# Optimization experiments

Measured on AMD Instinct MI355X. Metric: run time of the kernel, lower is better.

## Reference

```python
import jax, jax.numpy as jnp
import numpy as np

B, N, G, E = 4, 8192, 512, 512
D = 3 * E  # fused channel dim = 1536
BN_EPS = 1e-5


def setup_inputs() -> dict:
    key = jax.random.key(0)
    ks = jax.random.split(key, 8)
    f32 = jnp.float32
    return {
        "xyz": jax.random.normal(ks[0], (B, N, 3), f32),
        "centers": jax.random.normal(ks[1], (B, G, 3), f32),
        "H4": jax.random.normal(ks[2], (B, G, E), f32),
        "H8": jax.random.normal(ks[3], (B, G, E), f32),
        "H12": jax.random.normal(ks[4], (B, G, E), f32),
        "w1": jax.random.normal(ks[5], (512, D), f32) * 0.02,
        "b1": jnp.zeros((512,), f32),
        "g1": jnp.ones((512,), f32),
        "be1": jnp.zeros((512,), f32),
        "m1": jnp.zeros((512,), f32),
        "v1": jnp.ones((512,), f32),
        "w2": jax.random.normal(ks[6], (512, 512), f32) * 0.02,
        "b2": jnp.zeros((512,), f32),
        "g2": jnp.ones((512,), f32),
        "be2": jnp.zeros((512,), f32),
        "m2": jnp.zeros((512,), f32),
        "v2": jnp.ones((512,), f32),
    }


def _bn(x, gamma, beta, mean, var):
    # BatchNorm1d, eval mode with running stats (per-channel, last axis)
    return (x - mean) * jax.lax.rsqrt(var + BN_EPS) * gamma + beta


def reference(xyz, centers, H4, H8, H12,
              w1, b1, g1, be1, m1, v1,
              w2, b2, g2, be2, m2, v2):
    fused = jnp.concatenate([H4, H8, H12], axis=-1)  # [B,G,D]
    # squared pairwise distances [B,N,G]
    d = (jnp.sum(xyz * xyz, axis=-1, keepdims=True)
         + jnp.sum(centers * centers, axis=-1)[:, None, :]
         - 2.0 * jnp.einsum('bnc,bgc->bng', xyz, centers))
    neg_d3, idx = jax.lax.top_k(-d, 3)  # 3 smallest distances, ascending
    d3 = -neg_d3  # [B,N,3]
    recip = 1.0 / (d3 + 1e-8)
    w = recip / jnp.sum(recip, axis=-1, keepdims=True)  # [B,N,3]
    # gather neighbor features: [B,N,3,D]
    gathered = jax.vmap(lambda f, i: f[i])(fused, idx)
    interp = jnp.einsum('bnk,bnkd->bnd', w, gathered)  # [B,N,D]
    # 1x1 conv == per-point linear; conv -> BN(eval) -> ReLU, twice
    h = jax.nn.relu(_bn(interp @ w1.T + b1, g1, be1, m1, v1))
    h = jax.nn.relu(_bn(h @ w2.T + b2, g2, be2, m2, v2))
    return h  # [B,N,512]
```

## Files before the change

kernel.cpp:

```cpp
#include <hip/hip_runtime.h>
#include <hip/hip_cooperative_groups.h>
#include <stdint.h>

#define NP 8192
#define NG 512
#define DF 1536

namespace cg = cooperative_groups;

using f32x4    = __attribute__((ext_vector_type(4))) float;
using bf16x8   = __attribute__((ext_vector_type(8))) __bf16;
using ushort8v = __attribute__((ext_vector_type(8))) unsigned short;


__device__ __forceinline__ unsigned short f32_to_bf16(float f) {
  unsigned int u = __float_as_uint(f);
  u += 0x7fffu + ((u >> 16) & 1u);
  return (unsigned short)(u >> 16);
}
__device__ __forceinline__ float bf2f(unsigned short u) {
  return __uint_as_float(((unsigned)u) << 16);
}

struct FusedArgs {
  const float *xyz, *centers, *H4, *H8, *H12, *w1, *w2;
  const float *g1, *be1, *m1, *v1, *g2, *be2, *m2, *v2, *b1, *b2;
  unsigned short *fswz, *w1s, *w2s, *Amatb, *h1s;
  int *nidx; float *nw, *s1, *t1, *s2, *t2;
  float *outp;
};

__device__ void phase_setup(const FusedArgs& a, char* smem, int w) {
  const int tid = threadIdx.x;
  if (w < 512) {
    float4* cs = (float4*)smem;
    const int b = w >> 7;
    for (int i = tid; i < NG; i += 256) {
      float c0 = a.centers[((size_t)b * NG + i) * 3 + 0];
      float c1 = a.centers[((size_t)b * NG + i) * 3 + 1];
      float c2 = a.centers[((size_t)b * NG + i) * 3 + 2];
      float4 v; v.x = c0; v.y = c1; v.z = c2; v.w = c0 * c0 + c1 * c1 + c2 * c2;
      cs[(i >> 7) * 129 + (i & 127)] = v;
    }
    __syncthreads();
    const int t = (w & 127) * 256 + tid;
    const int p = t >> 2, q = t & 3;
    const size_t pi = (size_t)b * NP + p;
    const float x0 = a.xyz[pi * 3 + 0], x1 = a.xyz[pi * 3 + 1], x2 = a.xyz[pi * 3 + 2];
    const float xx = x0 * x0 + x1 * x1 + x2 * x2;
    float d0 = 3.4e38f, d1 = 3.4e38f, d2 = 3.4e38f;
    int i0 = 0, i1 = 0, i2 = 0;
    const int gbase = q * 128;
    const float4* csq = cs + q * 129;
#pragma unroll 4
    for (int j = 0; j < 128; ++j) {
      float4 c = csq[j];
      float d = xx + c.w - 2.0f * (x0 * c.x + x1 * c.y + x2 * c.z);
      int g = gbase + j;
      bool c0 = d < d0, c1 = d < d1, c2 = d < d2;
      float nd2 = c1 ? d1 : (c2 ? d : d2); int ni2 = c1 ? i1 : (c2 ? g : i2);
      float nd1 = c0 ? d0 : (c1 ? d : d1); int ni1 = c0 ? i0 : (c1 ? g : i1);
      d0 = c0 ? d : d0;                    i0 = c0 ? g : i0;
      d1 = nd1; i1 = ni1; d2 = nd2; i2 = ni2;
    }
#pragma unroll
    for (int off = 1; off <= 2; off <<= 1) {
      float e0 = __shfl_xor(d0, off), e1 = __shfl_xor(d1, off), e2 = __shfl_xor(d2, off);
      int j0 = __shfl_xor(i0, off), j1 = __shfl_xor(i1, off), j2 = __shfl_xor(i2, off);
#pragma unroll
      for (int s = 0; s < 3; ++s) {
        float e = (s == 0) ? e0 : (s == 1 ? e1 : e2);
        int   j = (s == 0) ? j0 : (s == 1 ? j1 : j2);
        bool c0 = (e < d0) || (e == d0 && j < i0);
        bool c1 = (e < d1) || (e == d1 && j < i1);
        bool c2 = (e < d2) || (e == d2 && j < i2);
        float nd2 = c1 ? d1 : (c2 ? e : d2); int ni2 = c1 ? i1 : (c2 ? j : i2);
        float nd1 = c0 ? d0 : (c1 ? e : d1); int ni1 = c0 ? i0 : (c1 ? j : i1);
        d0 = c0 ? e : d0;                    i0 = c0 ? j : i0;
        d1 = nd1; i1 = ni1; d2 = nd2; i2 = ni2;
      }
    }
    if (q == 0) {
      float r0 = 1.0f / (d0 + 1e-8f), r1 = 1.0f / (d1 + 1e-8f), r2 = 1.0f / (d2 + 1e-8f);
      float inv = 1.0f / (r0 + r1 + r2);
      a.nw[pi * 3 + 0] = r0 * inv; a.nw[pi * 3 + 1] = r1 * inv; a.nw[pi * 3 + 2] = r2 * inv;
      a.nidx[pi * 3 + 0] = i0; a.nidx[pi * 3 + 1] = i1; a.nidx[pi * 3 + 2] = i2;
    }
    __syncthreads();
  } else if (w < 2048) {
    const int qd = (w - 512) * 256 + tid;
    const int L = qd & 63, t2 = qd >> 6;
    const int kc = t2 % 48, mg = t2 / 48;
    const int m = mg * 16 + (L & 15);
    const int k = kc * 32 + (L >> 4) * 8;
    const float* src = (k < 512) ? a.H4 : (k < 1024 ? a.H8 : a.H12);
    const float* sp = &src[(size_t)m * 512 + (k & 511)];
    float4 va = *(const float4*)sp, vb = *(const float4*)(sp + 4);
    ushort8v o;
    o[0] = f32_to_bf16(va.x); o[1] = f32_to_bf16(va.y);
    o[2] = f32_to_bf16(va.z); o[3] = f32_to_bf16(va.w);
    o[4] = f32_to_bf16(vb.x); o[5] = f32_to_bf16(vb.y);
    o[6] = f32_to_bf16(vb.z); o[7] = f32_to_bf16(vb.w);
    *(ushort8v*)&a.fswz[((size_t)(mg * 48 + kc)) * 512 + L * 8] = o;
  } else if (w < 2432) {
    const int qd = (w - 2048) * 256 + tid;
    const int L = qd & 63, t2 = qd >> 6;
    const int kc = t2 % 48, ng = t2 / 48;
    const int n = ng * 16 + (L & 15);
    const int k = kc * 32 + (L >> 4) * 8;
    const float* sp = &a.w1[(size_t)n * 1536 + k];
    float4 va = *(const float4*)sp, vb = *(const float4*)(sp + 4);
    ushort8v o;
    o[0] = f32_to_bf16(va.x); o[1] = f32_to_bf16(va.y);
    o[2] = f32_to_bf16(va.z); o[3] = f32_to_bf16(va.w);
    o[4] = f32_to_bf16(vb.x); o[5] = f32_to_bf16(vb.y);
    o[6] = f32_to_bf16(vb.z); o[7] = f32_to_bf16(vb.w);
    *(ushort8v*)&a.w1s[((size_t)(ng * 48 + kc)) * 512 + L * 8] = o;
  } else if (w < 2560) {
    const int qd = (w - 2432) * 256 + tid;
    const int L = qd & 63, t2 = qd >> 6;
    const int kc = t2 & 15, ng = t2 >> 4;
    const int n = ng * 16 + (L & 15);
    const int k = kc * 32 + (L >> 4) * 8;
    const float* sp = &a.w2[(size_t)n * 512 + k];
    float4 va = *(const float4*)sp, vb = *(const float4*)(sp + 4);
    ushort8v o;
    o[0] = f32_to_bf16(va.x); o[1] = f32_to_bf16(va.y);
    o[2] = f32_to_bf16(va.z); o[3] = f32_to_bf16(va.w);
    o[4] = f32_to_bf16(vb.x); o[5] = f32_to_bf16(vb.y);
    o[6] = f32_to_bf16(vb.z); o[7] = f32_to_bf16(vb.w);
    *(ushort8v*)&a.w2s[((size_t)(ng * 16 + kc)) * 512 + L * 8] = o;
  } else {
    for (int i = tid; i < 512; i += 256) {
      float sa = a.g1[i] / sqrtf(a.v1[i] + 1e-5f);
      a.s1[i] = sa; a.t1[i] = a.be1[i] - a.m1[i] * sa;
      float sb = a.g2[i] / sqrtf(a.v2[i] + 1e-5f);
      a.s2[i] = sb; a.t2[i] = a.be2[i] - a.m2[i] * sb;
    }
  }
}

__device__ void phase_gemm1(const FusedArgs& a, char* smem) {
  float* red = (float*)smem;
  const int tid = threadIdx.x, lane = tid & 63, wv = tid >> 6;
  const int blk = blockIdx.x;
  const int m0 = (blk >> 3) * 32;
  const int n0 = (blk & 7) * 64;
  const unsigned short* Ap = a.fswz + ((size_t)(m0 >> 4) * 48 + wv * 12) * 512 + lane * 8;
  const unsigned short* Bp = a.w1s  + ((size_t)(n0 >> 4) * 48 + wv * 12) * 512 + lane * 8;

  f32x4 acc[2][4];
#pragma unroll
  for (int i = 0; i < 2; ++i)
#pragma unroll
    for (int j = 0; j < 4; ++j) acc[i][j] = (f32x4){0.f, 0.f, 0.f, 0.f};

  bf16x8 af[2], bfr[4], afn[2], bfn[4];
#pragma unroll
  for (int i = 0; i < 2; ++i)
    af[i]  = __builtin_bit_cast(bf16x8, *(const ushort8v*)(Ap + (size_t)i * 48 * 512));
#pragma unroll
  for (int i = 0; i < 4; ++i)
    bfr[i] = __builtin_bit_cast(bf16x8, *(const ushort8v*)(Bp + (size_t)i * 48 * 512));
#pragma unroll 1
  for (int kc = 0; kc < 12; ++kc) {
    if (kc < 11) {
#pragma unroll
      for (int i = 0; i < 2; ++i)
        afn[i] = __builtin_bit_cast(bf16x8, *(const ushort8v*)(Ap + (size_t)i * 48 * 512 + (kc + 1) * 512));
#pragma unroll
      for (int i = 0; i < 4; ++i)
        bfn[i] = __builtin_bit_cast(bf16x8, *(const ushort8v*)(Bp + (size_t)i * 48 * 512 + (kc + 1) * 512));
    }
#pragma unroll
    for (int mi = 0; mi < 2; ++mi)
#pragma unroll
      for (int ni = 0; ni < 4; ++ni)
        acc[mi][ni] = __builtin_amdgcn_mfma_f32_16x16x32_bf16(af[mi], bfr[ni], acc[mi][ni], 0, 0, 0);
#pragma unroll
    for (int i = 0; i < 2; ++i) af[i] = afn[i];
#pragma unroll
    for (int i = 0; i < 4; ++i) bfr[i] = bfn[i];
  }

  for (int w = 0; w < 4; ++w) {
    if (wv == w) {
#pragma unroll
      for (int mi = 0; mi < 2; ++mi)
#pragma unroll
        for (int ni = 0; ni < 4; ++ni) {
          int col = ni * 16 + (lane & 15);
#pragma unroll
          for (int r = 0; r < 4; ++r) {
            int row = mi * 16 + (lane >> 4) * 4 + r;
            if (w == 0) red[row * 65 + col] = acc[mi][ni][r];
            else        red[row * 65 + col] += acc[mi][ni][r];
          }
        }
    }
    __syncthreads();
  }
  const int row = tid >> 3;
  const int col = (tid & 7) * 8;
  ushort8v o;
#pragma unroll
  for (int j = 0; j < 8; ++j) {
    int n = n0 + col + j;
    float v = red[row * 65 + col + j];
    o[j] = f32_to_bf16(a.s1[n] * (v + a.b1[n]) + a.t1[n]);
  }
  *(ushort8v*)&a.Amatb[(size_t)(m0 + row) * 512 + n0 + col] = o;
}

__device__ void phase_interp(const FusedArgs& a) {
  const int tid = threadIdx.x, lane = tid & 63, wv = tid >> 6;
  const int pg = blockIdx.x * 4 + wv;
  const int p = pg * 16 + (lane & 15);
  const int b = p >> 13;
  const int i0 = a.nidx[p * 3 + 0], i1 = a.nidx[p * 3 + 1], i2 = a.nidx[p * 3 + 2];
  const float w0 = a.nw[p * 3 + 0], w1v = a.nw[p * 3 + 1], w2v = a.nw[p * 3 + 2];
  const unsigned short* A0 = a.Amatb + ((size_t)(b * 512 + i0)) * 512;
  const unsigned short* A1 = a.Amatb + ((size_t)(b * 512 + i1)) * 512;
  const unsigned short* A2 = a.Amatb + ((size_t)(b * 512 + i2)) * 512;
  const int cbase = (lane >> 4) * 8;
  unsigned short* wp = a.h1s + ((size_t)pg * 16) * 512 + lane * 8;
#pragma unroll 4
  for (int cc = 0; cc < 16; ++cc) {
    const int c = cc * 32 + cbase;
    ushort8v u0 = *(const ushort8v*)&A0[c];
    ushort8v u1 = *(const ushort8v*)&A1[c];
    ushort8v u2 = *(const ushort8v*)&A2[c];
    ushort8v o;
#pragma unroll
    for (int j = 0; j < 8; ++j) {
      float v = w0 * bf2f(u0[j]) + w1v * bf2f(u1[j]) + w2v * bf2f(u2[j]);
      o[j] = f32_to_bf16(fmaxf(v, 0.f));
    }
    *(ushort8v*)(wp + (size_t)cc * 512) = o;
  }
}

__device__ void phase_gemm2(const FusedArgs& a, int L) {
  const int tid = threadIdx.x, lane = tid & 63, wv = tid >> 6;
  const int wm = wv >> 1, wn = wv & 1;
  const int xcd = L & 7, slot = L >> 3;
  const int mloc = slot >> 2, nt = slot & 3;
  const int m0 = (xcd * 32 + mloc) * 128, n0 = nt * 128;

  const unsigned short* Ap = a.h1s + ((size_t)((m0 >> 4) + wm * 4) * 16) * 512 + lane * 8;
  const unsigned short* Bp = a.w2s + ((size_t)((n0 >> 4) + wn * 4) * 16) * 512 + lane * 8;

  f32x4 acc[4][4];
#pragma unroll
  for (int i = 0; i < 4; ++i)
#pragma unroll
    for (int j = 0; j < 4; ++j) acc[i][j] = (f32x4){0.f, 0.f, 0.f, 0.f};

  bf16x8 af[4], bfr[4], afn[4], bfn[4];
#pragma unroll
  for (int i = 0; i < 4; ++i) {
    af[i]  = __builtin_bit_cast(bf16x8, *(const ushort8v*)(Ap + (size_t)i * 16 * 512));
    bfr[i] = __builtin_bit_cast(bf16x8, *(const ushort8v*)(Bp + (size_t)i * 16 * 512));
  }
#pragma unroll 1
  for (int kc = 0; kc < 16; ++kc) {
    if (kc < 15) {
#pragma unroll
      for (int i = 0; i < 4; ++i) {
        afn[i] = __builtin_bit_cast(bf16x8, *(const ushort8v*)(Ap + (size_t)i * 16 * 512 + (kc + 1) * 512));
        bfn[i] = __builtin_bit_cast(bf16x8, *(const ushort8v*)(Bp + (size_t)i * 16 * 512 + (kc + 1) * 512));
      }
    }
#pragma unroll
    for (int mi = 0; mi < 4; ++mi)
#pragma unroll
      for (int ni = 0; ni < 4; ++ni)
        acc[mi][ni] = __builtin_amdgcn_mfma_f32_16x16x32_bf16(af[mi], bfr[ni], acc[mi][ni], 0, 0, 0);
#pragma unroll
    for (int i = 0; i < 4; ++i) { af[i] = afn[i]; bfr[i] = bfn[i]; }
  }

#pragma unroll
  for (int mi = 0; mi < 4; ++mi) {
    int mbase = m0 + wm * 64 + mi * 16 + (lane >> 4) * 4;
#pragma unroll
    for (int ni = 0; ni < 4; ++ni) {
      int n = n0 + wn * 64 + ni * 16 + (lane & 15);
      float s = a.s2[n], bb = a.b2[n], t = a.t2[n];
      f32x4 v = acc[mi][ni];
#pragma unroll
      for (int r = 0; r < 4; ++r) {
        float val = fmaxf(s * (v[r] + bb) + t, 0.f);
        a.outp[(size_t)(mbase + r) * 512 + n] = val;
      }
    }
  }
}

__global__ __launch_bounds__(256, 2) void fused_kernel(FusedArgs a) {
  __shared__ __align__(16) char smem[8448];
  cg::grid_group grid = cg::this_grid();
  const int blk = blockIdx.x;
  for (int u = blk; u <= 2560; u += 512) phase_setup(a, smem, u);
  grid.sync();
  phase_gemm1(a, smem);
  grid.sync();
  phase_interp(a);
  grid.sync();
  phase_gemm2(a, blk);
  phase_gemm2(a, blk + 512);
}

__global__ __launch_bounds__(256) void k_setup(FusedArgs a) {
  __shared__ __align__(16) char smem[8448];
  for (int u = blockIdx.x; u <= 2560; u += 512) phase_setup(a, smem, u);
}
__global__ __launch_bounds__(256) void k_gemm1(FusedArgs a) {
  __shared__ __align__(16) char smem[8448];
  phase_gemm1(a, smem);
}
__global__ __launch_bounds__(256) void k_interp(FusedArgs a) { phase_interp(a); }
__global__ __launch_bounds__(256) void k_gemm2(FusedArgs a) {
  phase_gemm2(a, blockIdx.x);
  phase_gemm2(a, blockIdx.x + 512);
}

extern "C" void kernel_launch(void* const* d_in, const int* in_sizes, int n_in,
                              void* d_out, int out_size, void* d_ws, size_t ws_size,
                              hipStream_t stream) {
  char* ws = (char*)d_ws;
  FusedArgs a;
  a.xyz     = (const float*)d_in[0];
  a.centers = (const float*)d_in[1];
  a.H4      = (const float*)d_in[2];
  a.H8      = (const float*)d_in[3];
  a.H12     = (const float*)d_in[4];
  a.w1      = (const float*)d_in[5];
  a.b1      = (const float*)d_in[6];
  a.g1      = (const float*)d_in[7];
  a.be1     = (const float*)d_in[8];
  a.m1      = (const float*)d_in[9];
  a.v1      = (const float*)d_in[10];
  a.w2      = (const float*)d_in[11];
  a.b2      = (const float*)d_in[12];
  a.g2      = (const float*)d_in[13];
  a.be2     = (const float*)d_in[14];
  a.m2      = (const float*)d_in[15];
  a.v2      = (const float*)d_in[16];
  a.fswz  = (unsigned short*)(ws);
  a.w1s   = (unsigned short*)(ws + 6291456);
  a.w2s   = (unsigned short*)(ws + 7864320);
  a.Amatb = (unsigned short*)(ws + 8388608);
  a.h1s   = (unsigned short*)(ws + 12582912);
  a.nidx  = (int*)           (ws + 46137344);
  a.nw    = (float*)         (ws + 46530560);
  a.s1    = (float*)         (ws + 46923776);
  a.t1 = a.s1 + 512; a.s2 = a.t1 + 512; a.t2 = a.s2 + 512;
  a.outp  = (float*)d_out;

  int nb = 0;
  hipError_t qerr = hipOccupancyMaxActiveBlocksPerMultiprocessor(
      &nb, reinterpret_cast<const void*>(fused_kernel), 256, 0);
  bool coop_ok = (qerr == hipSuccess) && (nb >= 2);
  if (coop_ok) {
    void* kp[] = { (void*)&a };
    hipError_t lerr = hipLaunchCooperativeKernel(
        (const void*)fused_kernel, dim3(512), dim3(256), kp, 0, stream);
    coop_ok = (lerr == hipSuccess);
  }
  if (!coop_ok) {
    k_setup <<<512, 256, 0, stream>>>(a);
    k_gemm1 <<<512, 256, 0, stream>>>(a);
    k_interp<<<512, 256, 0, stream>>>(a);
    k_gemm2 <<<512, 256, 0, stream>>>(a);
  }
}
```

Measured before the change: 178.0 us.

## Fuse interpolation into GEMM2 via shared memory, removing h1 global buffer

Merges the interpolation and second GEMM phases so each block interpolates its 64 points into a 64 KB LDS tile, then multiplies that tile against all 512 output channels with each wave covering 128 columns. This drops the bf16 h1 round trip through global memory and one grid-wide barrier. In exchange, each block now needs 64 KB of LDS, which may limit co-residency to two blocks per CU and could make the cooperative launch fail and fall back to the separate-kernel path. W2 fragments are also no longer prefetched across k steps, and LDS reads use a lane*8 stride that may cause bank conflicts.

```diff
diff --git a/kernel.cpp b/kernel.cpp
--- a/kernel.cpp
+++ b/kernel.cpp
@@ -25,7 +25,7 @@
 struct FusedArgs {
   const float *xyz, *centers, *H4, *H8, *H12, *w1, *w2;
   const float *g1, *be1, *m1, *v1, *g2, *be2, *m2, *v2, *b1, *b2;
-  unsigned short *fswz, *w1s, *w2s, *Amatb, *h1s;
+  unsigned short *fswz, *w1s, *w2s, *Amatb;
   int *nidx; float *nw, *s1, *t1, *s2, *t2;
   float *outp;
 };
@@ -210,105 +210,92 @@
     o[j] = f32_to_bf16(a.s1[n] * (v + a.b1[n]) + a.t1[n]);
   }
   *(ushort8v*)&a.Amatb[(size_t)(m0 + row) * 512 + n0 + col] = o;
-}
-
-__device__ void phase_interp(const FusedArgs& a) {
+  __syncthreads();
+}
+
+__device__ void phase_mega(const FusedArgs& a, char* smem) {
+  unsigned short* hl = (unsigned short*)smem;
   const int tid = threadIdx.x, lane = tid & 63, wv = tid >> 6;
-  const int pg = blockIdx.x * 4 + wv;
-  const int p = pg * 16 + (lane & 15);
-  const int b = p >> 13;
-  const int i0 = a.nidx[p * 3 + 0], i1 = a.nidx[p * 3 + 1], i2 = a.nidx[p * 3 + 2];
-  const float w0 = a.nw[p * 3 + 0], w1v = a.nw[p * 3 + 1], w2v = a.nw[p * 3 + 2];
-  const unsigned short* A0 = a.Amatb + ((size_t)(b * 512 + i0)) * 512;
-  const unsigned short* A1 = a.Amatb + ((size_t)(b * 512 + i1)) * 512;
-  const unsigned short* A2 = a.Amatb + ((size_t)(b * 512 + i2)) * 512;
-  const int cbase = (lane >> 4) * 8;
-  unsigned short* wp = a.h1s + ((size_t)pg * 16) * 512 + lane * 8;
+  const int xcd = blockIdx.x & 7, slot = blockIdx.x >> 3;
+  const int m0 = (xcd * 64 + slot) * 64;
+
+  {
+    const int p = m0 + wv * 16 + (lane & 15);
+    const int b = p >> 13;
+    const int i0 = a.nidx[p * 3 + 0], i1 = a.nidx[p * 3 + 1], i2 = a.nidx[p * 3 + 2];
+    const float w0 = a.nw[p * 3 + 0], w1v = a.nw[p * 3 + 1], w2v = a.nw[p * 3 + 2];
+    const int co = (lane >> 4) * 8;
+    const unsigned short* A0 = a.Amatb + ((size_t)(b * 512 + i0)) * 512 + co;
+    const unsigned short* A1 = a.Amatb + ((size_t)(b * 512 + i1)) * 512 + co;
+    const unsigned short* A2 = a.Amatb + ((size_t)(b * 512 + i2)) * 512 + co;
+    unsigned short* wp = hl + (size_t)(wv * 16) * 512 + lane * 8;
 #pragma unroll 4
-  for (int cc = 0; cc < 16; ++cc) {
-    const int c = cc * 32 + cbase;
-    ushort8v u0 = *(const ushort8v*)&A0[c];
-    ushort8v u1 = *(const ushort8v*)&A1[c];
-    ushort8v u2 = *(const ushort8v*)&A2[c];
-    ushort8v o;
-#pragma unroll
-    for (int j = 0; j < 8; ++j) {
-      float v = w0 * bf2f(u0[j]) + w1v * bf2f(u1[j]) + w2v * bf2f(u2[j]);
-      o[j] = f32_to_bf16(fmaxf(v, 0.f));
-    }
-    *(ushort8v*)(wp + (size_t)cc * 512) = o;
-  }
-}
-
-__device__ void phase_gemm2(const FusedArgs& a, int L) {
-  const int tid = threadIdx.x, lane = tid & 63, wv = tid >> 6;
-  const int wm = wv >> 1, wn = wv & 1;
-  const int xcd = L & 7, slot = L >> 3;
-  const int mloc = slot >> 2, nt = slot & 3;
-  const int m0 = (xcd * 32 + mloc) * 128, n0 = nt * 128;
-
-  const unsigned short* Ap = a.h1s + ((size_t)((m0 >> 4) + wm * 4) * 16) * 512 + lane * 8;
-  const unsigned short* Bp = a.w2s + ((size_t)((n0 >> 4) + wn * 4) * 16) * 512 + lane * 8;
-
-  f32x4 acc[4][4];
+    for (int kc = 0; kc < 16; ++kc) {
+      ushort8v u0 = *(const ushort8v*)(A0 + kc * 32);
+      ushort8v u1 = *(const ushort8v*)(A1 + kc * 32);
+      ushort8v u2 = *(const ushort8v*)(A2 + kc * 32);
+      ushort8v o;
+#pragma unroll
+      for (int j = 0; j < 8; ++j) {
+        float v = w0 * bf2f(u0[j]) + w1v * bf2f(u1[j]) + w2v * bf2f(u2[j]);
+        o[j] = f32_to_bf16(fmaxf(v, 0.f));
+      }
+      *(ushort8v*)(wp + (size_t)kc * 512) = o;
+    }
+  }
+  __syncthreads();
+
+  const int n0 = wv * 128;
+  const unsigned short* Bbase = a.w2s + (size_t)(n0 >> 4) * 16 * 512 + lane * 8;
+
+  f32x4 acc[4][8];
 #pragma unroll
   for (int i = 0; i < 4; ++i)
 #pragma unroll
-    for (int j = 0; j < 4; ++j) acc[i][j] = (f32x4){0.f, 0.f, 0.f, 0.f};
-
-  bf16x8 af[4], bfr[4], afn[4], bfn[4];
-#pragma unroll
-  for (int i = 0; i < 4; ++i) {
-    af[i]  = __builtin_bit_cast(bf16x8, *(const ushort8v*)(Ap + (size_t)i * 16 * 512));
-    bfr[i] = __builtin_bit_cast(bf16x8, *(const ushort8v*)(Bp + (size_t)i * 16 * 512));
-  }
+    for (int j = 0; j < 8; ++j) acc[i][j] = (f32x4){0.f, 0.f, 0.f, 0.f};
+
 #pragma unroll 1
   for (int kc = 0; kc < 16; ++kc) {
-    if (kc < 15) {
-#pragma unroll
-      for (int i = 0; i < 4; ++i) {
-        afn[i] = __builtin_bit_cast(bf16x8, *(const ushort8v*)(Ap + (size_t)i * 16 * 512 + (kc + 1) * 512));
-        bfn[i] = __builtin_bit_cast(bf16x8, *(const ushort8v*)(Bp + (size_t)i * 16 * 512 + (kc + 1) * 512));
-      }
-    }
+    bf16x8 af[4], bfr[8];
 #pragma unroll
     for (int mi = 0; mi < 4; ++mi)
-#pragma unroll
-      for (int ni = 0; ni < 4; ++ni)
+      af[mi] = __builtin_bit_cast(bf16x8,
+          *(const ushort8v*)(hl + (size_t)(mi * 16 + kc) * 512 + lane * 8));
+#pragma unroll
+    for (int ni = 0; ni < 8; ++ni)
+      bfr[ni] = __builtin_bit_cast(bf16x8,
+          *(const ushort8v*)(Bbase + (size_t)(ni * 16 + kc) * 512));
+#pragma unroll
+    for (int mi = 0; mi < 4; ++mi)
+#pragma unroll
+      for (int ni = 0; ni < 8; ++ni)
         acc[mi][ni] = __builtin_amdgcn_mfma_f32_16x16x32_bf16(af[mi], bfr[ni], acc[mi][ni], 0, 0, 0);
-#pragma unroll
-    for (int i = 0; i < 4; ++i) { af[i] = afn[i]; bfr[i] = bfn[i]; }
   }
 
 #pragma unroll
   for (int mi = 0; mi < 4; ++mi) {
-    int mbase = m0 + wm * 64 + mi * 16 + (lane >> 4) * 4;
-#pragma unroll
-    for (int ni = 0; ni < 4; ++ni) {
-      int n = n0 + wn * 64 + ni * 16 + (lane & 15);
+    int mbase = m0 + mi * 16 + (lane >> 4) * 4;
+#pragma unroll
+    for (int ni = 0; ni < 8; ++ni) {
+      int n = n0 + ni * 16 + (lane & 15);
       float s = a.s2[n], bb = a.b2[n], t = a.t2[n];
       f32x4 v = acc[mi][ni];
 #pragma unroll
-      for (int r = 0; r < 4; ++r) {
-        float val = fmaxf(s * (v[r] + bb) + t, 0.f);
-        a.outp[(size_t)(mbase + r) * 512 + n] = val;
-      }
+      for (int r = 0; r < 4; ++r)
+        a.outp[(size_t)(mbase + r) * 512 + n] = fmaxf(s * (v[r] + bb) + t, 0.f);
     }
   }
 }
 
 __global__ __launch_bounds__(256, 2) void fused_kernel(FusedArgs a) {
-  __shared__ __align__(16) char smem[8448];
+  __shared__ __align__(16) char smem[65536];
   cg::grid_group grid = cg::this_grid();
   const int blk = blockIdx.x;
   for (int u = blk; u <= 2560; u += 512) phase_setup(a, smem, u);
   grid.sync();
   phase_gemm1(a, smem);
   grid.sync();
-  phase_interp(a);
-  grid.sync();
-  phase_gemm2(a, blk);
-  phase_gemm2(a, blk + 512);
+  phase_mega(a, smem);
 }
 
 __global__ __launch_bounds__(256) void k_setup(FusedArgs a) {
@@ -319,10 +306,9 @@
   __shared__ __align__(16) char smem[8448];
   phase_gemm1(a, smem);
 }
-__global__ __launch_bounds__(256) void k_interp(FusedArgs a) { phase_interp(a); }
-__global__ __launch_bounds__(256) void k_gemm2(FusedArgs a) {
-  phase_gemm2(a, blockIdx.x);
-  phase_gemm2(a, blockIdx.x + 512);
+__global__ __launch_bounds__(256, 2) void k_mega(FusedArgs a) {
+  __shared__ __align__(16) char smem[65536];
+  phase_mega(a, smem);
 }
 
 extern "C" void kernel_launch(void* const* d_in, const int* in_sizes, int n_in,
@@ -351,10 +337,9 @@
   a.w1s   = (unsigned short*)(ws + 6291456);
   a.w2s   = (unsigned short*)(ws + 7864320);
   a.Amatb = (unsigned short*)(ws + 8388608);
-  a.h1s   = (unsigned short*)(ws + 12582912);
-  a.nidx  = (int*)           (ws + 46137344);
-  a.nw    = (float*)         (ws + 46530560);
-  a.s1    = (float*)         (ws + 46923776);
+  a.nidx  = (int*)           (ws + 10485760);
+  a.nw    = (float*)         (ws + 10878976);
+  a.s1    = (float*)         (ws + 11272192);
   a.t1 = a.s1 + 512; a.s2 = a.t1 + 512; a.t2 = a.s2 + 512;
   a.outp  = (float*)d_out;
 
@@ -371,7 +356,6 @@
   if (!coop_ok) {
     k_setup <<<512, 256, 0, stream>>>(a);
     k_gemm1 <<<512, 256, 0, stream>>>(a);
-    k_interp<<<512, 256, 0, stream>>>(a);
-    k_gemm2 <<<512, 256, 0, stream>>>(a);
-  }
-}
+    k_mega  <<<512, 256, 0, stream>>>(a);
+  }
+}
```

New measurement: 166.8 us. -6.3%, faster.
